# Optimization experiments

Hardware: AMD Instinct MI355X
Metric: run time of the kernel (lower is better)

The kernel has to match this reference:

```python
import jax, jax.numpy as jnp
import numpy as np

B, T, HID, OUT = 8, 256, 256, 6
DT = 0.1

def setup_inputs() -> dict:
    key = jax.random.key(0)
    ks = jax.random.split(key, 16)
    n = lambda i, shp, s: jax.random.normal(ks[i], shp, jnp.float32) * s
    return {
        "frames": jax.random.normal(ks[0], (B, T, 3, 64, 64), jnp.float32),
        "hidden_state": jnp.zeros((B, HID), jnp.float32),
        "conv1_w": n(1, (32, 3, 3, 3), 0.2), "conv1_b": jnp.zeros((32,), jnp.float32),
        "conv2_w": n(2, (64, 32, 3, 3), 0.1), "conv2_b": jnp.zeros((64,), jnp.float32),
        "conv3_w": n(3, (128, 64, 3, 3), 0.1), "conv3_b": jnp.zeros((128,), jnp.float32),
        "enc_w": n(4, (HID, 128), 0.08), "enc_b": jnp.zeros((HID,), jnp.float32),
        "ltc_wr": n(5, (HID, HID), 0.05), "ltc_wi": n(6, (HID, HID), 0.05),
        "ltc_b": jnp.zeros((HID,), jnp.float32),
        "ltc_tau": jax.random.uniform(ks[7], (HID,), jnp.float32, 0.5, 1.5),
        "ltc_a": n(8, (HID,), 1.0),
        "dec_w1": n(9, (128, HID), 0.08), "dec_b1": jnp.zeros((128,), jnp.float32),
        "dec_w2": n(10, (64, 128), 0.1), "dec_b2": jnp.zeros((64,), jnp.float32),
        "dec_w3": n(11, (OUT, 64), 0.1), "dec_b3": jnp.zeros((OUT,), jnp.float32),
    }

def _conv(x, w, b):
    y = jax.lax.conv_general_dilated(x, w, (2, 2), [(1, 1), (1, 1)],
                                     dimension_numbers=("NCHW", "OIHW", "NCHW"))
    return y + b[None, :, None, None]

def reference(frames, hidden_state, conv1_w, conv1_b, conv2_w, conv2_b, conv3_w, conv3_b,
              enc_w, enc_b, ltc_wr, ltc_wi, ltc_b, ltc_tau, ltc_a,
              dec_w1, dec_b1, dec_w2, dec_b2, dec_w3, dec_b3):
    Bb, Tt = frames.shape[:2]
    x = frames.reshape(Bb * Tt, 3, 64, 64)
    x = jax.nn.relu(_conv(x, conv1_w, conv1_b))   # (BT,32,32,32)
    x = jax.nn.relu(_conv(x, conv2_w, conv2_b))   # (BT,64,16,16)
    x = jax.nn.relu(_conv(x, conv3_w, conv3_b))   # (BT,128,8,8); adaptive pool to (8,8) is identity here
    feats = x.reshape(Bb, Tt, 128, 8, 8).transpose(0, 1, 3, 4, 2).reshape(Bb, Tt, 64, 128)
    node = feats @ enc_w.T + enc_b                # (B,T,64,HID)
    x_seq = node.mean(axis=2).transpose(1, 0, 2)  # (T,B,HID)

    def step(h, x_t):
        # LTC Euler update, dt=0.1, n_steps=1
        f = jnp.tanh(h @ ltc_wr.T + x_t @ ltc_wi.T + ltc_b)
        h_new = h + DT * (-(1.0 / ltc_tau + f) * h + f * ltc_a)
        y = jax.nn.relu(h_new @ dec_w1.T + dec_b1)
        y = jax.nn.relu(y @ dec_w2.T + dec_b2)
        c = y @ dec_w3.T + dec_b3
        return h_new, c

    final_hidden, controls = jax.lax.scan(step, hidden_state, x_seq)
    return controls.transpose(1, 0, 2), final_hidden
```

## Files before the change

kernel.cpp:

```cpp
#include <hip/hip_runtime.h>

#define T_STEPS 256
#define B_SZ 8
#define HID 256

typedef _Float16 hv2 __attribute__((ext_vector_type(2)));
typedef _Float16 f16x4 __attribute__((ext_vector_type(4)));
typedef float f32x4 __attribute__((ext_vector_type(4)));
union H2U { hv2 h; unsigned u; };
union U2F { uint2 u; f16x4 h; };
__device__ inline hv2 u2h(unsigned u){ H2U c; c.u = u; return c.h; }
__device__ inline unsigned h2u(hv2 h){ H2U c; c.h = h; return c.u; }
__device__ inline hv2 relu2(hv2 v){
  unsigned u = h2u(v);
  unsigned s = (u & 0x80008000u) >> 15;
  u &= ~(s * 0xFFFFu);
  return u2h(u);
}
__device__ inline unsigned packh2f(float lo, float hi){
  hv2 h; h.x = (_Float16)lo; h.y = (_Float16)hi; return h2u(h);
}

#define OFF_XW   0
#define OFF_HH   524288
#define OFF_WFT  1141760
#define OFF_BF   1174528
#define OFF_D1T  1174784
#define OFF_D2T  1207552
#define OFF_D3T  1215744
#define OFF_W1P  1216128
#define OFF_W2F  1216560
#define OFF_W3F  1225776
#define OFF_WRP  1262640

__global__ __launch_bounds__(256) void prep_kernel(
    const float* __restrict__ conv1_w, const float* __restrict__ conv2_w,
    const float* __restrict__ conv3_w, const float* __restrict__ enc_w,
    const float* __restrict__ enc_b,  const float* __restrict__ ltc_wi,
    const float* __restrict__ ltc_b,  const float* __restrict__ ltc_wr,
    const float* __restrict__ dec_w1,
    const float* __restrict__ dec_w2, const float* __restrict__ dec_w3,
    float* __restrict__ ws)
{
  int gtid = blockIdx.x * 256 + threadIdx.x;
  int nth = gridDim.x * 256;
  unsigned* wsu = (unsigned*)ws;
  for (int e = gtid; e < 128 * 256; e += nth) {
    int j = e >> 7, m = e & 127;
    float s = 0.f;
    for (int k = 0; k < 256; ++k) s = fmaf(ltc_wi[j*256 + k], enc_w[k*128 + m], s);
    ws[OFF_WFT + m*256 + j] = s;
  }
  for (int e = gtid; e < 256; e += nth) {
    float s = ltc_b[e];
    for (int k = 0; k < 256; ++k) s = fmaf(ltc_wi[e*256 + k], enc_b[k], s);
    ws[OFF_BF + e] = s;
  }
  for (int e = gtid; e < 27*16; e += nth) { int k = e>>4, p = e&15;
    wsu[OFF_W1P+e] = packh2f(conv1_w[(2*p)*27 + k], conv1_w[(2*p+1)*27 + k]); }
  for (int e = gtid; e < 9216; e += nth) {
    int dpair = e & 1;
    int tmp = e >> 1;
    int l = tmp & 63; tmp >>= 6;
    int nt = tmp & 3; tmp >>= 2;
    int kt = tmp % 9, hp = tmp / 9;
    int oc = nt*16 + (l & 15);
    int ic = hp*16 + ((l>>4)<<2) + (dpair<<1);
    int ky = kt/3, kx = kt%3;
    wsu[OFF_W2F + e] = packh2f(conv2_w[((oc*32 + ic)*3 + ky)*3 + kx],
                               conv2_w[((oc*32 + ic+1)*3 + ky)*3 + kx]);
  }
  for (int e = gtid; e < 36864; e += nth) {
    int dpair = e & 1;
    int tmp = e >> 1;
    int l = tmp & 63; tmp >>= 6;
    int nt = tmp & 7; tmp >>= 3;
    int kt = tmp;
    int kyx = kt >> 2;
    int ky = kyx/3, kx = kyx%3;
    int ic = ((kt & 3) << 4) + ((l>>4)<<2) + (dpair<<1);
    int oc = nt*16 + (l & 15);
    wsu[OFF_W3F + e] = packh2f(conv3_w[((oc*64 + ic)*3 + ky)*3 + kx],
                               conv3_w[((oc*64 + ic+1)*3 + ky)*3 + kx]);
  }
  for (int e = gtid; e < 32768; e += nth) {
    int i = e & 31;
    int j = (e >> 5) & 255;
    int q = e >> 13;
    wsu[OFF_WRP + e] = packh2f(ltc_wr[j*256 + q*64 + 2*i],
                               ltc_wr[j*256 + q*64 + 2*i + 1]);
  }
  for (int e = gtid; e < 256*128;e += nth) { int k = e>>7, i = e&127; ws[OFF_D1T+e] = dec_w1[i*256 + k]; }
  for (int e = gtid; e < 128*64; e += nth) { int k = e>>6, i = e&63;  ws[OFF_D2T+e] = dec_w2[i*128 + k]; }
  for (int e = gtid; e < 64*6;   e += nth) { int k = e/6,  o = e%6;   ws[OFF_D3T+e] = dec_w3[o*64 + k]; }
}

__global__ __launch_bounds__(256, 3) void enc_kernel(
    const float* __restrict__ frames,
    const float* __restrict__ b1, const float* __restrict__ b2,
    const float* __restrict__ b3, float* __restrict__ ws)
{
  extern __shared__ __align__(16) unsigned lds[];
  unsigned* buf0  = lds;
  unsigned* w3buf = lds + 8192;
  unsigned* w1s   = lds + 12288;
  float* fmp = (float*)(lds + 12720);

  const int tid = threadIdx.x;
  const int l   = tid & 63;
  const int w   = tid >> 6;
  const int kg  = l >> 4;
  const int lc  = l & 15;
  const int bt  = blockIdx.x;
  const int b   = bt >> 8, t = bt & 255;
  const float* fr = frames + (size_t)bt * 12288;
  const unsigned* wsu = (const unsigned*)ws;
  const uint2* w2f = (const uint2*)(wsu + OFF_W2F);
  const uint4* w3src = (const uint4*)(wsu + OFF_W3F);

  if (tid < 216) ((uint2*)w1s)[tid] = ((const uint2*)(wsu + OFF_W1P))[tid];
  __syncthreads();

  f32x4 acc2[4][4];
  #pragma unroll
  for (int mi = 0; mi < 4; ++mi)
    #pragma unroll
    for (int nt = 0; nt < 4; ++nt) {
      float bb = b2[nt*16 + lc];
      acc2[mi][nt] = (f32x4){bb, bb, bb, bb};
    }

  for (int hp = 0; hp < 2; ++hp) {
    for (int p = 0; p < 4; ++p) {
      int pos = p*256 + tid;
      int y = pos >> 5, x = pos & 31;
      hv2 a1[8];
      #pragma unroll
      for (int o = 0; o < 8; ++o) { a1[o].x = (_Float16)b1[16*hp+2*o]; a1[o].y = (_Float16)b1[16*hp+2*o+1]; }
      for (int ic = 0; ic < 3; ++ic)
        for (int ky = 0; ky < 3; ++ky) {
          int iy = 2*y - 1 + ky;
          bool rok = (unsigned)iy < 64u;
          for (int kx = 0; kx < 3; ++kx) {
            int ix = 2*x - 1 + kx;
            float v = (rok && (unsigned)ix < 64u) ? fr[ic*4096 + iy*64 + ix] : 0.f;
            _Float16 hf = (_Float16)v;
            hv2 vs; vs.x = hf; vs.y = hf;
            int k = ic*9 + ky*3 + kx;
            uint4 wa = ((uint4*)w1s)[k*4 + hp*2];
            uint4 wb = ((uint4*)w1s)[k*4 + hp*2 + 1];
            a1[0] = vs * u2h(wa.x) + a1[0];
            a1[1] = vs * u2h(wa.y) + a1[1];
            a1[2] = vs * u2h(wa.z) + a1[2];
            a1[3] = vs * u2h(wa.w) + a1[3];
            a1[4] = vs * u2h(wb.x) + a1[4];
            a1[5] = vs * u2h(wb.y) + a1[5];
            a1[6] = vs * u2h(wb.z) + a1[6];
            a1[7] = vs * u2h(wb.w) + a1[7];
          }
        }
      unsigned r0 = h2u(relu2(a1[0])), r1 = h2u(relu2(a1[1]));
      unsigned r2 = h2u(relu2(a1[2])), r3 = h2u(relu2(a1[3]));
      unsigned r4 = h2u(relu2(a1[4])), r5 = h2u(relu2(a1[5]));
      unsigned r6 = h2u(relu2(a1[6])), r7 = h2u(relu2(a1[7]));
      int s = pos & 3;
      uint4 v0, v1;
      if (s & 1) { v0 = make_uint4(r2,r3,r0,r1); v1 = make_uint4(r6,r7,r4,r5); }
      else       { v0 = make_uint4(r0,r1,r2,r3); v1 = make_uint4(r4,r5,r6,r7); }
      int sl = (s >> 1) & 1;
      ((uint4*)buf0)[pos*2 + sl]     = v0;
      ((uint4*)buf0)[pos*2 + (1^sl)] = v1;
    }
    __syncthreads();
    #pragma unroll
    for (int ky = 0; ky < 3; ++ky)
      #pragma unroll
      for (int kx = 0; kx < 3; ++kx) {
        int kt = ky*3 + kx;
        U2F bf[4];
        #pragma unroll
        for (int nt = 0; nt < 4; ++nt)
          bf[nt].u = w2f[(((hp*9 + kt)*4 + nt)<<6) + l];
        #pragma unroll
        for (int mi = 0; mi < 4; ++mi) {
          int mt = w*4 + mi;
          int iy = 2*mt - 1 + ky;
          if (iy >= 0) {
            int ix = 2*lc - 1 + kx;
            bool okx = (unsigned)ix < 32u;
            int pos1 = iy*32 + (okx ? ix : 0);
            U2F av; av.u = ((const uint2*)buf0)[pos1*4 + (kg ^ (pos1 & 3))];
            if (!okx) { av.u.x = 0u; av.u.y = 0u; }
            #pragma unroll
            for (int nt = 0; nt < 4; ++nt)
              acc2[mi][nt] = __builtin_amdgcn_mfma_f32_16x16x16f16(av.h, bf[nt].h, acc2[mi][nt], 0, 0, 0);
          }
        }
      }
    __syncthreads();
  }

  {
    uint4 s0a = w3src[tid];
    uint4 s0b = w3src[256 + tid];
    _Float16* act2h = (_Float16*)buf0;
    #pragma unroll
    for (int mi = 0; mi < 4; ++mi)
      #pragma unroll
      for (int nt = 0; nt < 4; ++nt)
        #pragma unroll
        for (int i = 0; i < 4; ++i) {
          int pos = (w*4 + mi)*16 + 4*kg + i;
          int oc = nt*16 + lc;
          float vv = fmaxf(acc2[mi][nt][i], 0.f);
          int ocp = (((oc >> 2) ^ (pos & 7)) << 2) + (oc & 3);
          act2h[pos*64 + ocp] = (_Float16)vv;
        }
    ((uint4*)w3buf)[tid] = s0a;
    ((uint4*)w3buf)[256 + tid] = s0b;
  }

  f32x4 acc3[8];
  #pragma unroll
  for (int nt = 0; nt < 8; ++nt) { float bb = b3[nt*16 + lc]; acc3[nt] = (f32x4){bb, bb, bb, bb}; }
  const int y3 = (w*16 + lc) >> 3, x3 = lc & 7;
  __syncthreads();

  for (int cc = 0; cc < 18; ++cc) {
    uint4 st0, st1;
    if (cc < 17) {
      st0 = w3src[(cc+1)*512 + tid];
      st1 = w3src[(cc+1)*512 + 256 + tid];
    }
    int kyx = cc >> 1;
    int ky = kyx / 3, kx = kyx % 3;
    int iy = 2*y3 - 1 + ky, ix = 2*x3 - 1 + kx;
    bool ok = ((unsigned)iy < 16u) && ((unsigned)ix < 16u);
    int posIn = (ok ? iy : 0)*16 + (ok ? ix : 0);
    int sw = posIn & 7;
    const uint2* bvp = (const uint2*)w3buf + (cc & 1)*1024;
    #pragma unroll
    for (int k2 = 0; k2 < 2; ++k2) {
      int kt = 2*cc + k2;
      int icb = (kt & 3)*4 + kg;
      U2F av; av.u = ((const uint2*)buf0)[posIn*16 + (icb ^ sw)];
      if (!ok) { av.u.x = 0u; av.u.y = 0u; }
      #pragma unroll
      for (int nt = 0; nt < 8; ++nt) {
        U2F bv; bv.u = bvp[((k2*8 + nt)<<6) + l];
        acc3[nt] = __builtin_amdgcn_mfma_f32_16x16x16f16(av.h, bv.h, acc3[nt], 0, 0, 0);
      }
    }
    if (cc < 17) {
      ((uint4*)w3buf)[((cc+1)&1)*512 + tid] = st0;
      ((uint4*)w3buf)[((cc+1)&1)*512 + 256 + tid] = st1;
    }
    __syncthreads();
  }

  #pragma unroll
  for (int nt = 0; nt < 8; ++nt) {
    float s = 0.f;
    #pragma unroll
    for (int i = 0; i < 4; ++i) s += fmaxf(acc3[nt][i], 0.f);
    s += __shfl_xor(s, 16);
    s += __shfl_xor(s, 32);
    if (l < 16) fmp[w*128 + nt*16 + l] = s;
  }
  __syncthreads();
  if (tid < 128) {
    float s = fmp[tid] + fmp[128 + tid] + fmp[256 + tid] + fmp[384 + tid];
    fmp[tid] = s * (1.f/64.f);
  }
  __syncthreads();
  {
    float accx = ws[OFF_BF + tid];
    const float* wfT = ws + OFF_WFT;
    for (int m = 0; m < 128; ++m) accx = fmaf(fmp[m], wfT[m*256 + tid], accx);
    ws[OFF_XW + (t*B_SZ + b)*HID + tid] = accx;
  }
}

__global__ __launch_bounds__(1024) void scan_kernel(
    const float* __restrict__ tau, const float* __restrict__ av,
    const float* __restrict__ h0,
    float* __restrict__ ws, float* __restrict__ outh)
{
  const int b = blockIdx.x;
  const int tid = threadIdx.x;
  const int j = tid & 255, q = tid >> 8;
  __shared__ float hf[256];
  __shared__ unsigned hp16[128];
  __shared__ float part[4][256];
  __shared__ float hbuf[16*256];

  uint4 wv[8];
  {
    const uint4* wp = (const uint4*)((const unsigned*)ws + OFF_WRP + (q*256 + j)*32);
    #pragma unroll
    for (int r = 0; r < 8; ++r) wv[r] = wp[r];
  }
  const float tinv = 1.f / tau[j];
  const float aj = av[j];
  const float* xw = ws + OFF_XW;
  float* hh = ws + OFF_HH;

  {
    float hv0 = h0[b*256 + j];
    float hvn = __shfl_xor(hv0, 1);
    if (q == 0) {
      hf[j] = hv0;
      if (!(j & 1)) hp16[j >> 1] = packh2f(hv0, hvn);
    }
  }
  float xw_pref = xw[(0*B_SZ + b)*HID + j];
  __syncthreads();

  for (int t = 0; t < T_STEPS; ++t) {
    float xwv = xw_pref;
    xw_pref = xw[((t+1)*B_SZ + b)*HID + j];
    hv2 acc = {(_Float16)0.f, (_Float16)0.f};
    const uint4* hq = (const uint4*)hp16 + q*8;
    #pragma unroll
    for (int r = 0; r < 8; ++r) {
      uint4 hvp = hq[r];
      acc = u2h(hvp.x) * u2h(wv[r].x) + acc;
      acc = u2h(hvp.y) * u2h(wv[r].y) + acc;
      acc = u2h(hvp.z) * u2h(wv[r].z) + acc;
      acc = u2h(hvp.w) * u2h(wv[r].w) + acc;
    }
    float hv0 = hf[j];
    part[q][j] = (float)acc.x + (float)acc.y;
    __syncthreads();
    float pre = part[0][j] + part[1][j] + part[2][j] + part[3][j] + xwv;
    float f = 1.f - 2.f / (1.f + __expf(2.f * pre));
    float hn = fmaf(0.1f, fmaf(-(tinv + f), hv0, f * aj), hv0);
    float hnn = __shfl_xor(hn, 1);
    if (q == 0) {
      hf[j] = hn;
      hbuf[(t & 15)*256 + j] = hn;
      if (!(j & 1)) hp16[j >> 1] = packh2f(hn, hnn);
    }
    __syncthreads();
    if ((t & 15) == 15) {
      int base = t - 15;
      int st = tid >> 6;
      int col = (tid & 63) << 2;
      *(float4*)(hh + ((base + st)*B_SZ + b)*HID + col) = *(float4*)(hbuf + st*256 + col);
    }
  }
  if (q == 0) outh[b*HID + j] = hf[j];
}

__global__ __launch_bounds__(256) void dec_kernel(
    const float* __restrict__ db1, const float* __restrict__ db2,
    const float* __restrict__ db3, const float* __restrict__ ws,
    float* __restrict__ outc)
{
  const int bid = blockIdx.x;
  const int b = bid >> 8, t = bid & 255;
  const int tid = threadIdx.x;
  __shared__ float hloc[256];
  __shared__ float p1[2][128];
  __shared__ float y1s[128];
  __shared__ float p2[4][64];
  __shared__ float y2s[64];
  const float* hh  = ws + OFF_HH + (t*B_SZ + b)*HID;
  const float* d1T = ws + OFF_D1T;
  const float* d2T = ws + OFF_D2T;
  const float* d3T = ws + OFF_D3T;
  hloc[tid] = hh[tid];
  __syncthreads();
  {
    int i = tid & 127, hf = tid >> 7;
    float s = 0.f;
    for (int k = hf*128; k < hf*128 + 128; ++k) s = fmaf(hloc[k], d1T[k*128 + i], s);
    p1[hf][i] = s;
  }
  __syncthreads();
  if (tid < 128) y1s[tid] = fmaxf(p1[0][tid] + p1[1][tid] + db1[tid], 0.f);
  __syncthreads();
  {
    int i = tid & 63, r = tid >> 6;
    float s = 0.f;
    for (int k = r*32; k < r*32 + 32; ++k) s = fmaf(y1s[k], d2T[k*64 + i], s);
    p2[r][i] = s;
  }
  __syncthreads();
  if (tid < 64) y2s[tid] = fmaxf(p2[0][tid] + p2[1][tid] + p2[2][tid] + p2[3][tid] + db2[tid], 0.f);
  __syncthreads();
  if (tid < 6) {
    float s = db3[tid];
    for (int k = 0; k < 64; ++k) s = fmaf(y2s[k], d3T[k*6 + tid], s);
    outc[(b*T_STEPS + t)*6 + tid] = s;
  }
}

extern "C" void kernel_launch(void* const* d_in, const int* in_sizes, int n_in,
                              void* d_out, int out_size, void* d_ws, size_t ws_size,
                              hipStream_t stream)
{
  const float* frames = (const float*)d_in[0];
  const float* h0   = (const float*)d_in[1];
  const float* c1w  = (const float*)d_in[2];
  const float* c1b  = (const float*)d_in[3];
  const float* c2w  = (const float*)d_in[4];
  const float* c2b  = (const float*)d_in[5];
  const float* c3w  = (const float*)d_in[6];
  const float* c3b  = (const float*)d_in[7];
  const float* encw = (const float*)d_in[8];
  const float* encb = (const float*)d_in[9];
  const float* wr   = (const float*)d_in[10];
  const float* wi   = (const float*)d_in[11];
  const float* lb   = (const float*)d_in[12];
  const float* ltau = (const float*)d_in[13];
  const float* la   = (const float*)d_in[14];
  const float* dw1  = (const float*)d_in[15];
  const float* db1  = (const float*)d_in[16];
  const float* dw2  = (const float*)d_in[17];
  const float* db2  = (const float*)d_in[18];
  const float* dw3  = (const float*)d_in[19];
  const float* db3  = (const float*)d_in[20];
  float* out = (float*)d_out;
  float* ws  = (float*)d_ws;

  hipLaunchKernelGGL(prep_kernel, dim3(256), dim3(256), 0, stream,
                     c1w, c2w, c3w, encw, encb, wi, lb, wr, dw1, dw2, dw3, ws);
  hipLaunchKernelGGL(enc_kernel, dim3(2048), dim3(256), 52928, stream,
                     frames, c1b, c2b, c3b, ws);
  hipLaunchKernelGGL(scan_kernel, dim3(B_SZ), dim3(1024), 0, stream,
                     ltau, la, h0, ws, out + 12288);
  hipLaunchKernelGGL(dec_kernel, dim3(2048), dim3(256), 0, stream,
                     db1, db2, db3, ws, out);
}
```

Measured before the change: 503.2 us.

## Stage frames as padded fp16 in LDS for conv1 and vectorize conv2 weight loads

Each frame is now loaded once with coalesced float4 reads and converted to fp16 into a zero-padded LDS tile. conv1 then reads from LDS with fully unrolled loops and no bounds checks, instead of making scattered, predicated global loads that re-read each pixel several times and twice across the hp loop. The conv2 weight layout is permuted so each lane fetches its four B fragments with two uint4 loads. LDS use grows to about 65KB, so launch_bounds drops from 3 to 2 blocks per SM, which lowers occupancy.

```diff
diff --git a/kernel.cpp b/kernel.cpp
--- a/kernel.cpp
+++ b/kernel.cpp
@@ -32,6 +32,8 @@
 #define OFF_W2F  1216560
 #define OFF_W3F  1225776
 #define OFF_WRP  1262640
+
+#define ENC_LDS_DW 16264
 
 __global__ __launch_bounds__(256) void prep_kernel(
     const float* __restrict__ conv1_w, const float* __restrict__ conv2_w,
@@ -60,10 +62,10 @@
     wsu[OFF_W1P+e] = packh2f(conv1_w[(2*p)*27 + k], conv1_w[(2*p+1)*27 + k]); }
   for (int e = gtid; e < 9216; e += nth) {
     int dpair = e & 1;
-    int tmp = e >> 1;
-    int l = tmp & 63; tmp >>= 6;
-    int nt = tmp & 3; tmp >>= 2;
-    int kt = tmp % 9, hp = tmp / 9;
+    int nt = (e >> 1) & 3;
+    int l  = (e >> 3) & 63;
+    int g  = e >> 9;
+    int kt = g % 9, hp = g / 9;
     int oc = nt*16 + (l & 15);
     int ic = hp*16 + ((l>>4)<<2) + (dpair<<1);
     int ky = kt/3, kx = kt%3;
@@ -95,16 +97,18 @@
   for (int e = gtid; e < 64*6;   e += nth) { int k = e/6,  o = e%6;   ws[OFF_D3T+e] = dec_w3[o*64 + k]; }
 }
 
-__global__ __launch_bounds__(256, 3) void enc_kernel(
+__global__ __launch_bounds__(256, 2) void enc_kernel(
     const float* __restrict__ frames,
     const float* __restrict__ b1, const float* __restrict__ b2,
     const float* __restrict__ b3, float* __restrict__ ws)
 {
   extern __shared__ __align__(16) unsigned lds[];
   unsigned* buf0  = lds;
+  unsigned* frH   = lds + 8192;
   unsigned* w3buf = lds + 8192;
-  unsigned* w1s   = lds + 12288;
-  float* fmp = (float*)(lds + 12720);
+  unsigned* w1s   = lds + 15320;
+  float* fmp = (float*)(lds + 15752);
+  _Float16* frHh = (_Float16*)frH;
 
   const int tid = threadIdx.x;
   const int l   = tid & 63;
@@ -115,10 +119,30 @@
   const int b   = bt >> 8, t = bt & 255;
   const float* fr = frames + (size_t)bt * 12288;
   const unsigned* wsu = (const unsigned*)ws;
-  const uint2* w2f = (const uint2*)(wsu + OFF_W2F);
+  const uint4* w2f4 = (const uint4*)(wsu + OFF_W2F);
   const uint4* w3src = (const uint4*)(wsu + OFF_W3F);
 
-  if (tid < 216) ((uint2*)w1s)[tid] = ((const uint2*)(wsu + OFF_W1P))[tid];
+  {
+    uint4 z4 = make_uint4(0u, 0u, 0u, 0u);
+    for (int i = tid; i < 1782; i += 256) ((uint4*)frH)[i] = z4;
+    if (tid < 216) ((uint2*)w1s)[tid] = ((const uint2*)(wsu + OFF_W1P))[tid];
+  }
+  __syncthreads();
+  {
+    const float4* fr4 = (const float4*)fr;
+    #pragma unroll
+    for (int p = 0; p < 12; ++p) {
+      int fidx = p*256 + tid;
+      float4 v = fr4[fidx];
+      int ic = fidx >> 10, rem = fidx & 1023;
+      int iy = rem >> 4, xq = rem & 15;
+      int dw = ic*2376 + (iy+1)*36 + 2*xq + 2;
+      uint2 pk;
+      pk.x = packh2f(v.x, v.y);
+      pk.y = packh2f(v.z, v.w);
+      *(uint2*)(frH + dw) = pk;
+    }
+  }
   __syncthreads();
 
   f32x4 acc2[4][4];
@@ -134,17 +158,17 @@
     for (int p = 0; p < 4; ++p) {
       int pos = p*256 + tid;
       int y = pos >> 5, x = pos & 31;
+      int base = 2*y*72 + 2*x;
       hv2 a1[8];
       #pragma unroll
       for (int o = 0; o < 8; ++o) { a1[o].x = (_Float16)b1[16*hp+2*o]; a1[o].y = (_Float16)b1[16*hp+2*o+1]; }
+      #pragma unroll
       for (int ic = 0; ic < 3; ++ic)
-        for (int ky = 0; ky < 3; ++ky) {
-          int iy = 2*y - 1 + ky;
-          bool rok = (unsigned)iy < 64u;
+        #pragma unroll
+        for (int ky = 0; ky < 3; ++ky)
+          #pragma unroll
           for (int kx = 0; kx < 3; ++kx) {
-            int ix = 2*x - 1 + kx;
-            float v = (rok && (unsigned)ix < 64u) ? fr[ic*4096 + iy*64 + ix] : 0.f;
-            _Float16 hf = (_Float16)v;
+            _Float16 hf = frHh[base + ic*4752 + ky*72 + kx + 3];
             hv2 vs; vs.x = hf; vs.y = hf;
             int k = ic*9 + ky*3 + kx;
             uint4 wa = ((uint4*)w1s)[k*4 + hp*2];
@@ -158,7 +182,6 @@
             a1[6] = vs * u2h(wb.z) + a1[6];
             a1[7] = vs * u2h(wb.w) + a1[7];
           }
-        }
       unsigned r0 = h2u(relu2(a1[0])), r1 = h2u(relu2(a1[1]));
       unsigned r2 = h2u(relu2(a1[2])), r3 = h2u(relu2(a1[3]));
       unsigned r4 = h2u(relu2(a1[4])), r5 = h2u(relu2(a1[5]));
@@ -177,10 +200,14 @@
       #pragma unroll
       for (int kx = 0; kx < 3; ++kx) {
         int kt = ky*3 + kx;
+        int bidx = ((hp*9 + kt)*64 + l)*2;
+        uint4 q0 = w2f4[bidx];
+        uint4 q1 = w2f4[bidx + 1];
         U2F bf[4];
-        #pragma unroll
-        for (int nt = 0; nt < 4; ++nt)
-          bf[nt].u = w2f[(((hp*9 + kt)*4 + nt)<<6) + l];
+        bf[0].u = make_uint2(q0.x, q0.y);
+        bf[1].u = make_uint2(q0.z, q0.w);
+        bf[2].u = make_uint2(q1.x, q1.y);
+        bf[3].u = make_uint2(q1.z, q1.w);
         #pragma unroll
         for (int mi = 0; mi < 4; ++mi) {
           int mt = w*4 + mi;
@@ -426,7 +453,7 @@
 
   hipLaunchKernelGGL(prep_kernel, dim3(256), dim3(256), 0, stream,
                      c1w, c2w, c3w, encw, encb, wi, lb, wr, dw1, dw2, dw3, ws);
-  hipLaunchKernelGGL(enc_kernel, dim3(2048), dim3(256), 52928, stream,
+  hipLaunchKernelGGL(enc_kernel, dim3(2048), dim3(256), ENC_LDS_DW*4, stream,
                      frames, c1b, c2b, c3b, ws);
   hipLaunchKernelGGL(scan_kernel, dim3(B_SZ), dim3(1024), 0, stream,
                      ltau, la, h0, ws, out + 12288);
```

Result: faster. 408.5 us (-18.8%).
